# Kernel tuning notes

Measured on AMD Instinct MI355X. Metric: run time of the kernel, lower is better.

Reference implementation:

```python
import jax, jax.numpy as jnp
import numpy as np

NPERSEG = 512
STEP = 256
NSEG = 9            # frames for L=2048 with boundary='zeros', padded=True
NFREQ = 257
NUM_FILTER = 2
PI = 3.1415926      # same constant as source

_win = 0.5 * (1.0 - jnp.cos(2.0 * jnp.pi * jnp.arange(NPERSEG, dtype=jnp.float32) / NPERSEG))  # periodic hann (scipy get_window('hann'))
_win_sum = 256.0    # sum of periodic hann, exact


def _stft(x):
    # x: (B, D, L) real -> scipy.signal.stft(..., nperseg=512, noverlap=256) => (B, D, 257, 9)
    xp = jnp.pad(x, ((0, 0), (0, 0), (STEP, STEP)))  # boundary='zeros'
    idx = jnp.arange(NSEG)[:, None] * STEP + jnp.arange(NPERSEG)[None, :]
    frames = xp[..., idx] * _win                     # (B,D,9,512)
    Z = jnp.fft.rfft(frames, axis=-1) / _win_sum     # scaling='spectrum'
    return jnp.swapaxes(Z, -1, -2)                   # (B,D,257,9)


def _istft(Z):
    # Z: (B,D,257,9) complex -> (B,D,2048) real (scipy.signal.istft inverse)
    xs = jnp.fft.irfft(jnp.swapaxes(Z, -1, -2) * _win_sum, n=NPERSEG, axis=-1) * _win  # (B,D,9,512)
    total = NPERSEG + (NSEG - 1) * STEP  # 2560
    idx = (jnp.arange(NSEG)[:, None] * STEP + jnp.arange(NPERSEG)[None, :]).reshape(-1)
    B, D = Z.shape[0], Z.shape[1]
    x = jnp.zeros((B, D, total), xs.dtype).at[..., idx].add(xs.reshape(B, D, -1))
    norm = jnp.zeros((total,), jnp.float32).at[idx].add(jnp.tile(_win ** 2, NSEG))
    x = x / jnp.where(norm > 1e-10, norm, 1.0)
    return x[..., STEP:total - STEP]  # trim boundary padding -> length 2048


def _cplx(p):
    return p[..., 0] + 1j * p[..., 1]  # torch.view_as_complex


def _filter(x, length, bank):
    # x: (B,S,D) complex; bank: (K,S,D,2). power = x*x/length (complex square, as in source)
    power = x * x / length
    k = jnp.arange(NUM_FILTER, dtype=jnp.float32)
    coef = jnp.cos((2.0 * (k + 1.0) - 1.0) * PI / 2.0 * NUM_FILTER)  # matches source precedence
    return jnp.sum(power[None] * _cplx(bank)[:, None] * coef[:, None, None, None], axis=0)


def _ln(x, g, b):
    m = jnp.mean(x, -1, keepdims=True)
    v = jnp.mean((x - m) ** 2, -1, keepdims=True)
    return (x - m) * jax.lax.rsqrt(v + 1e-5) * g + b


def _addnorm(x, g1, b1, w1, bb1, w2, bb2, g2, b2):
    x = _ln(x, g1, b1)
    h = jax.nn.gelu(x @ w1.T + bb1, approximate=False)  # torch GELU (exact)
    return _ln(h @ w2.T + bb2 + x, g2, b2)


def setup_inputs() -> dict:
    key = jax.random.key(0)
    ks = jax.random.split(key, 12)
    B, D = 8, 768
    d = {}
    d['ecg'] = jax.random.normal(ks[0], (B, 2048, D), jnp.float32)
    d['image'] = jax.random.normal(ks[1], (B, 196, D), jnp.float32)
    d['ecg_filter_bank'] = jax.random.normal(ks[2], (2, 2313, D, 2), jnp.float32)
    d['cxr_filter_bank'] = jax.random.normal(ks[3], (2, 99, D, 2), jnp.float32)
    d['gate_sel'] = jax.random.normal(ks[4], (99, D, 2), jnp.float32)
    d['gate_w'] = jax.random.normal(ks[5], (D, D), jnp.float32) * 0.02
    d['gate_b'] = jnp.zeros((D,), jnp.float32)
    for i, p in enumerate(['e', 'c']):
        d[p + '_ln1_g'] = jnp.ones((D,), jnp.float32)
        d[p + '_ln1_b'] = jnp.zeros((D,), jnp.float32)
        d[p + '_w1'] = jax.random.normal(ks[6 + 2 * i], (D, D), jnp.float32) * 0.02
        d[p + '_b1'] = jnp.zeros((D,), jnp.float32)
        d[p + '_w2'] = jax.random.normal(ks[7 + 2 * i], (D, D), jnp.float32) * 0.02
        d[p + '_b2'] = jnp.zeros((D,), jnp.float32)
        d[p + '_ln2_g'] = jnp.ones((D,), jnp.float32)
        d[p + '_ln2_b'] = jnp.zeros((D,), jnp.float32)
    return d


def reference(ecg, image, ecg_filter_bank, cxr_filter_bank, gate_sel, gate_w, gate_b,
              e_ln1_g, e_ln1_b, e_w1, e_b1, e_w2, e_b2, e_ln2_g, e_ln2_b,
              c_ln1_g, c_ln1_b, c_w1, c_b1, c_w2, c_b2, c_ln2_g, c_ln2_b):
    B, S, D = ecg.shape
    N = image.shape[1]
    # STFT path (source detaches to CPU -> stop_gradient)
    Z = _stft(jnp.swapaxes(jax.lax.stop_gradient(ecg), 1, 2))       # (B,D,257,9)
    _ecg = jnp.transpose(Z, (0, 2, 3, 1)).reshape(B, NFREQ * NSEG, D)
    _img = jnp.fft.rfft(image, axis=1, norm='ortho')                # (B,99,D)
    _ecg = _filter(_ecg, NFREQ * NSEG, ecg_filter_bank)
    _img = _filter(_img, N // 2 + 1, cxr_filter_bank)
    # Cxr2EcgGate: complex selection, avgpool over spatial (real part), 1x1 conv
    gate = jnp.mean((_img * _cplx(gate_sel)).real, axis=1) @ gate_w.T + gate_b  # (B,D)
    ecg_g = _ecg * gate[:, None, :]
    # NOTE: source overwrites gated image with irfft of filtered _image (ecg_gate output unused)
    img_t = jnp.fft.irfft(_img, n=N, axis=1, norm='ortho')          # (B,N,D)
    Zg = jnp.transpose(ecg_g.reshape(B, NFREQ, NSEG, D), (0, 3, 1, 2))
    ecg_t = jnp.swapaxes(_istft(jax.lax.stop_gradient(Zg)), 1, 2)   # (B,2048,D); source detaches before istft
    text = _addnorm(ecg_t + ecg, e_ln1_g, e_ln1_b, e_w1, e_b1, e_w2, e_b2, e_ln2_g, e_ln2_b)
    img = _addnorm(img_t + image, c_ln1_g, c_ln1_b, c_w1, c_b1, c_w2, c_b2, c_ln2_g, c_ln2_b)
    return (text, img)
```

## Files before the change

kernel.cpp:

```cpp
#include <hip/hip_runtime.h>
#include <math.h>

namespace {

constexpr int B_ = 8;
constexpr int S_ = 2048;
constexpr int D_ = 768;
constexpr int N_ = 196;
constexpr int NF_ = 99;
constexpr int NFREQ_ = 257;
constexpr int NSEG_ = 9;
constexpr int NBINS_ = NFREQ_ * NSEG_;
constexpr int NW_ = D_ * D_;
constexpr float TWOPI_ = 6.28318530717958647692f;

using bf16x8 = __attribute__((ext_vector_type(8))) short;
using f32x4  = __attribute__((ext_vector_type(4))) float;

__device__ __forceinline__ int rev9(int x) { return (int)(__brev((unsigned)x) >> 23); }
__device__ __forceinline__ int padz(int i) { return i + (i >> 4); }

__device__ __forceinline__ unsigned short f2bf(float x) {
  unsigned u = __float_as_uint(x);
  u = (u + 0x7FFFu + ((u >> 16) & 1u)) >> 16;
  return (unsigned short)u;
}
__device__ __forceinline__ float bf2f(unsigned short h) {
  return __uint_as_float(((unsigned)h) << 16);
}

__device__ __forceinline__ float gelu_f(float v) {
  const float x = fabsf(v) * 0.70710678118654752440f;
  const float t = 1.0f / fmaf(0.3275911f, x, 1.0f);
  float p = fmaf(fmaf(fmaf(fmaf(1.061405429f, t, -1.453152027f), t, 1.421413741f),
                      t, -0.284496736f), t, 0.254829592f);
  const float e = __expf(-x * x);
  const float er = 1.0f - p * t * e;
  return 0.5f * v * (1.0f + ((v < 0.f) ? -er : er));
}

__device__ __forceinline__ void gload16(const void* g, void* l) {
  __builtin_amdgcn_global_load_lds((const __attribute__((address_space(1))) void*)g,
                                   (__attribute__((address_space(3))) void*)l, 16, 0, 0);
}

__device__ __forceinline__ float2 cmulf(float2 a, float2 b) {
  return make_float2(a.x * b.x - a.y * b.y, a.x * b.y + a.y * b.x);
}
__device__ __forceinline__ float2 cadd(float2 a, float2 b) {
  return make_float2(a.x + b.x, a.y + b.y);
}
__device__ __forceinline__ float2 csub(float2 a, float2 b) {
  return make_float2(a.x - b.x, a.y - b.y);
}

__global__ __launch_bounds__(256) void k_transpose_g(const float* __restrict__ src,
                                                     float* __restrict__ dst,
                                                     int R, int C) {
  __shared__ float tile[32][33];
  const int b = blockIdx.z;
  const int c0 = blockIdx.x * 32;
  const int r0 = blockIdx.y * 32;
  const int tx = threadIdx.x & 31, ty = threadIdx.x >> 5;
  for (int i = ty; i < 32; i += 8)
    tile[i][tx] = src[((size_t)b * R + r0 + i) * C + c0 + tx];
  __syncthreads();
  for (int i = ty; i < 32; i += 8)
    dst[((size_t)b * C + c0 + i) * R + r0 + tx] = tile[tx][i];
}

constexpr int PREP_W = (NW_ + 255) / 256;
constexpr int PREP_WALL = 4 * PREP_W;
__global__ __launch_bounds__(256) void k_prep(
    const float* __restrict__ w0, const float* __restrict__ w1,
    const float* __restrict__ w2, const float* __restrict__ w3,
    unsigned short* __restrict__ wbf, float2* __restrict__ twg,
    float2* __restrict__ twN) {
  const int bid = blockIdx.x;
  if (bid < PREP_WALL) {
    const int m = bid / PREP_W;
    const int i = (bid - m * PREP_W) * 256 + threadIdx.x;
    if (i >= NW_) return;
    const float* src = (m == 0) ? w0 : (m == 1) ? w1 : (m == 2) ? w2 : w3;
    wbf[(size_t)m * NW_ + i] = f2bf(src[i]);
  } else if (bid < PREP_WALL + 2) {
    const int i = (bid - PREP_WALL) * 256 + threadIdx.x;
    if (i >= 511) return;
    const int v = i + 1;
    const int h = 1 << (31 - __clz(v));
    const int j = v - h;
    float sn, cs;
    sincosf((float)j * ((TWOPI_ * 0.5f) / (float)h), &sn, &cs);
    twg[i] = make_float2(cs, sn);
  } else {
    const int i = threadIdx.x;
    if (i >= N_) return;
    float sn, cs;
    sincosf(TWOPI_ * (float)i / (float)N_, &sn, &cs);
    twN[i] = make_float2(cs, sn);
  }
}

__global__ __launch_bounds__(256) void k_fc_t(const float2* __restrict__ e2,
                                              float2* __restrict__ FcT) {
  __shared__ float2 tile[32][33];
  const int d0 = blockIdx.x * 32;
  const int k0 = blockIdx.y * 32;
  const int f = blockIdx.z;
  const int tx = threadIdx.x & 31, ty = threadIdx.x >> 5;
  for (int i = ty; i < 32; i += 8) {
    const int k = k0 + i;
    if (k < NFREQ_) {
      const size_t s = (size_t)(k * 9 + f) * D_ + d0 + tx;
      const float2 a = e2[s];
      const float2 b = e2[(size_t)NBINS_ * D_ + s];
      tile[i][tx] = make_float2(-(a.x + b.x), -(a.y + b.y));
    }
  }
  __syncthreads();
  const int k = k0 + tx;
  if (k < NFREQ_) {
    for (int i = ty; i < 32; i += 8)
      FcT[(size_t)(d0 + i) * NBINS_ + f * 257 + k] = tile[tx][i];
  }
}

__global__ __launch_bounds__(256) void k_img_dft_f(
    const float* __restrict__ image, const float2* __restrict__ bank2,
    const float2* __restrict__ gsel2, const float2* __restrict__ twN,
    float2* __restrict__ imgF, float* __restrict__ part) {
  const int fg = blockIdx.x;
  const int f0 = fg * 9;
  const int d = blockIdx.y * 256 + threadIdx.x;
  const int b = blockIdx.z;
  __shared__ float2 tws[9 * N_];
  for (int idx = threadIdx.x; idx < 9 * N_; idx += 256) {
    const int fi = idx / N_;
    const int t = idx - fi * N_;
    tws[idx] = twN[((f0 + fi) * t) % N_];
  }
  __syncthreads();
  float re[9] = {}, im[9] = {};
  const float* ip = image + (size_t)b * N_ * D_ + d;
  for (int t = 0; t < N_; ++t) {
    const float v = ip[(size_t)t * D_];
#pragma unroll
    for (int fi = 0; fi < 9; ++fi) {
      const float2 w = tws[fi * N_ + t];
      re[fi] = fmaf(v, w.x, re[fi]);
      im[fi] = fmaf(-v, w.y, im[fi]);
    }
  }
  const float sc = 1.0f / (196.0f * 99.0f);
  float gp = 0.f;
#pragma unroll
  for (int fi = 0; fi < 9; ++fi) {
    const int f = f0 + fi;
    const float pr = (re[fi] * re[fi] - im[fi] * im[fi]) * sc;
    const float pi2 = (2.f * re[fi] * im[fi]) * sc;
    const size_t fd = (size_t)f * D_ + d;
    const float2 c0 = bank2[fd];
    const float2 c1 = bank2[(size_t)NF_ * D_ + fd];
    const float fcr = -(c0.x + c1.x), fci = -(c0.y + c1.y);
    const float zr = pr * fcr - pi2 * fci;
    const float zi = pr * fci + pi2 * fcr;
    imgF[(size_t)(b * NF_ + f) * D_ + d] = make_float2(zr, zi);
    const float2 gw = gsel2[fd];
    gp += zr * gw.x - zi * gw.y;
  }
  part[((size_t)b * 11 + fg) * D_ + d] = gp;
}

__global__ __launch_bounds__(256) void k_gate_mm2(const float* __restrict__ part,
                                                  const float* __restrict__ W,
                                                  const float* __restrict__ bias,
                                                  float* __restrict__ gate) {
  __shared__ float row[8][D_];
  __shared__ float red[16][16][8];
  const int tid = threadIdx.x;
  const int d0 = blockIdx.x * 16;
  for (int i = tid; i < 8 * D_; i += 256) {
    const int b = i / D_, e = i - b * D_;
    float s = 0.f;
    for (int p = 0; p < 11; ++p) s += part[((size_t)b * 11 + p) * D_ + e];
    row[b][e] = s * (1.0f / 99.0f);
  }
  __syncthreads();
  const int dl = tid >> 4;
  const int ec = tid & 15;
  const float* w = W + (size_t)(d0 + dl) * D_ + ec * 48;
  float acc[8] = {};
  for (int e = 0; e < 48; e += 4) {
    const float4 wv = *reinterpret_cast<const float4*>(w + e);
    const int eg = ec * 48 + e;
#pragma unroll
    for (int b = 0; b < 8; ++b) {
      acc[b] = fmaf(row[b][eg], wv.x, acc[b]);
      acc[b] = fmaf(row[b][eg + 1], wv.y, acc[b]);
      acc[b] = fmaf(row[b][eg + 2], wv.z, acc[b]);
      acc[b] = fmaf(row[b][eg + 3], wv.w, acc[b]);
    }
  }
#pragma unroll
  for (int b = 0; b < 8; ++b) red[dl][ec][b] = acc[b];
  __syncthreads();
  if (tid < 128) {
    const int dl2 = tid >> 3, b = tid & 7;
    float s = bias[d0 + dl2];
    for (int c = 0; c < 16; ++c) s += red[dl2][c][b];
    gate[b * D_ + d0 + dl2] = s;
  }
}

__global__ __launch_bounds__(256) void k_img_idft(
    const float2* __restrict__ imgF, const float* __restrict__ image,
    const float2* __restrict__ twN, float* __restrict__ xi) {
  const int t0 = blockIdx.x * 14;
  const int d = blockIdx.y * 256 + threadIdx.x;
  const int b = blockIdx.z;
  __shared__ float2 tws[14 * NF_];
  for (int idx = threadIdx.x; idx < 14 * NF_; idx += 256) {
    const int ti = idx / NF_;
    const int f = idx - ti * NF_;
    tws[idx] = twN[((t0 + ti) * f) % N_];
  }
  __syncthreads();
  const float2* zp = imgF + (size_t)b * NF_ * D_ + d;
  const float2 z0 = zp[0];
  const float2 zny = zp[(size_t)(NF_ - 1) * D_];
  float acc[14];
#pragma unroll
  for (int ti = 0; ti < 14; ++ti)
    acc[ti] = z0.x + (((t0 + ti) & 1) ? -zny.x : zny.x);
  for (int f = 1; f < NF_ - 1; ++f) {
    const float2 z = zp[(size_t)f * D_];
#pragma unroll
    for (int ti = 0; ti < 14; ++ti) {
      const float2 w = tws[ti * NF_ + f];
      acc[ti] += 2.f * (z.x * w.x - z.y * w.y);
    }
  }
#pragma unroll
  for (int ti = 0; ti < 14; ++ti) {
    const size_t idx = (size_t)(b * N_ + t0 + ti) * D_ + d;
    xi[idx] = acc[ti] * (1.0f / 14.0f) + image[idx];
  }
}

__global__ __launch_bounds__(256) void k_layernorm_f2b(const float* __restrict__ x,
                                                       const float* __restrict__ g,
                                                       const float* __restrict__ b,
                                                       unsigned short* __restrict__ out) {
  const int row = blockIdx.x;
  const int tid = threadIdx.x;
  const float* xr = x + (size_t)row * D_;
  const float v0 = xr[tid], v1 = xr[tid + 256], v2 = xr[tid + 512];
  float s = v0 + v1 + v2;
  float q = v0 * v0 + v1 * v1 + v2 * v2;
  __shared__ float red[8];
  for (int off = 32; off > 0; off >>= 1) {
    s += __shfl_down(s, off);
    q += __shfl_down(q, off);
  }
  if ((tid & 63) == 0) { red[tid >> 6] = s; red[4 + (tid >> 6)] = q; }
  __syncthreads();
  s = red[0] + red[1] + red[2] + red[3];
  q = red[4] + red[5] + red[6] + red[7];
  const float mean = s * (1.0f / 768.0f);
  const float var = q * (1.0f / 768.0f) - mean * mean;
  const float inv = rsqrtf(var + 1e-5f);
  unsigned short* orow = out + (size_t)row * D_;
  orow[tid]       = f2bf((v0 - mean) * inv * g[tid]       + b[tid]);
  orow[tid + 256] = f2bf((v1 - mean) * inv * g[tid + 256] + b[tid + 256]);
  orow[tid + 512] = f2bf((v2 - mean) * inv * g[tid + 512] + b[tid + 512]);
}

template <int H, int DIR, bool TRIV>
__device__ __forceinline__ void pass8(float2* z, int l,
                                      float2 wa, float2 wb, float2 wc) {
  asm volatile("s_waitcnt lgkmcnt(0)" ::: "memory");
  const float sg = (DIR < 0) ? -1.f : 1.f;
  const int base = (H == 1) ? (l << 3)
                 : (H == 8) ? (((l >> 3) << 6) | (l & 7))
                            : l;
  const float2 x0 = z[padz(base)],         x1 = z[padz(base + H)];
  const float2 x2 = z[padz(base + 2 * H)], x3 = z[padz(base + 3 * H)];
  const float2 x4 = z[padz(base + 4 * H)], x5 = z[padz(base + 5 * H)];
  const float2 x6 = z[padz(base + 6 * H)], x7 = z[padz(base + 7 * H)];
  const float2 WA = make_float2(wa.x, sg * wa.y);
  const float2 WB = make_float2(wb.x, sg * wb.y);
  const float2 WC = make_float2(wc.x, sg * wc.y);
  const float2 WBp = make_float2(-sg * WB.y, sg * WB.x);
  float2 t, u;
  t = TRIV ? x1 : cmulf(x1, WA); const float2 A0 = cadd(x0, t), A1 = csub(x0, t);
  t = TRIV ? x3 : cmulf(x3, WA); const float2 A2 = cadd(x2, t), A3 = csub(x2, t);
  t = TRIV ? x5 : cmulf(x5, WA); const float2 A4 = cadd(x4, t), A5 = csub(x4, t);
  t = TRIV ? x7 : cmulf(x7, WA); const float2 A6 = cadd(x6, t), A7 = csub(x6, t);
  t = TRIV ? A2 : cmulf(A2, WB);
  u = TRIV ? make_float2(-sg * A3.y, sg * A3.x) : cmulf(A3, WBp);
  const float2 B0 = cadd(A0, t), B2 = csub(A0, t);
  const float2 B1 = cadd(A1, u), B3 = csub(A1, u);
  t = TRIV ? A6 : cmulf(A6, WB);
  u = TRIV ? make_float2(-sg * A7.y, sg * A7.x) : cmulf(A7, WBp);
  const float2 B4 = cadd(A4, t), B6 = csub(A4, t);
  const float2 B5 = cadd(A5, u), B7 = csub(A5, u);
  const float r_ = 0.70710678118654752440f;
  const float2 F1 = TRIV ? make_float2(r_, sg * r_)
                         : cmulf(WC, make_float2(r_, sg * r_));
  const float2 F2 = TRIV ? make_float2(0.f, sg)
                         : make_float2(-sg * WC.y, sg * WC.x);
  const float2 F3 = TRIV ? make_float2(-r_, sg * r_)
                         : cmulf(WC, make_float2(-r_, sg * r_));
  t = TRIV ? B4 : cmulf(B4, WC);
  z[padz(base)]         = cadd(B0, t);
  z[padz(base + 4 * H)] = csub(B0, t);
  t = cmulf(B5, F1);
  z[padz(base + H)]     = cadd(B1, t);
  z[padz(base + 5 * H)] = csub(B1, t);
  t = cmulf(B6, F2);
  z[padz(base + 2 * H)] = cadd(B2, t);
  z[padz(base + 6 * H)] = csub(B2, t);
  t = cmulf(B7, F3);
  z[padz(base + 3 * H)] = cadd(B3, t);
  z[padz(base + 7 * H)] = csub(B3, t);
}

template <int FA, int FB>
__device__ __forceinline__ void scatter_buf(float2* z, const float (&s)[8],
                                            float wlo, float whi, int rlo, int rhi) {
  constexpr int iAlo = (FA > 0) ? FA - 1 : 0;
  constexpr int iAhi = (FA < 8) ? FA : 0;
  constexpr int iBlo = (FB > 0) ? FB - 1 : 0;
  constexpr int iBhi = (FB >= 0 && FB < 8) ? FB : 0;
  const float aLo = (FA == 0) ? 0.f : s[iAlo] * wlo;
  const float aHi = (FA == 8) ? 0.f : s[iAhi] * whi;
  const float bLo = (FB <= 0) ? 0.f : s[iBlo] * wlo;
  const float bHi = (FB < 0 || FB == 8) ? 0.f : s[iBhi] * whi;
  z[rlo] = make_float2(aLo, bLo);
  z[rhi] = make_float2(aHi, bHi);
}

template <int FA, int FB>
__device__ __forceinline__ void filt_pack(const float2* z, int k, float g,
                                          float2 cA, float2 cB,
                                          float2& Ck, float2& Cm) {
  const int q = (512 - k) & 511;
  const float2 Zk = z[padz(k)], Zq = z[padz(q)];
  const float sc = 0.5f / 256.f;
  const float ar = (Zk.x + Zq.x) * sc, ai = (Zk.y - Zq.y) * sc;
  float yar, yai, ybr = 0.f, ybi = 0.f;
  {
    const float pr = (ar * ar - ai * ai) * (1.f / 2313.f);
    const float pi = (2.f * ar * ai) * (1.f / 2313.f);
    yar = (pr * cA.x - pi * cA.y) * g;
    yai = (pr * cA.y + pi * cA.x) * g;
  }
  if (FB >= 0) {
    const float br = (Zk.y + Zq.y) * sc, bi = (Zq.x - Zk.x) * sc;
    const float pr = (br * br - bi * bi) * (1.f / 2313.f);
    const float pi = (2.f * br * bi) * (1.f / 2313.f);
    ybr = (pr * cB.x - pi * cB.y) * g;
    ybi = (pr * cB.y + pi * cB.x) * g;
  }
  if (k == 0 || k == 256) {
    Ck = make_float2(yar, ybr);
    Cm = Ck;
  } else {
    Ck = make_float2(yar - ybi, yai + ybr);
    Cm = make_float2(yar + ybi, ybr - yai);
  }
}

template <int FA0, int FB0, int FA1, int FB1, int FA2, int FB2, int FA3, int FB3,
          int NBUF>
__device__ __forceinline__ void ecg_super4(int tid, float g,
                                           const float2* __restrict__ fc,
                                           const float (&s)[8], const float2 (&ptw)[6],
                                           float2 t8, float2* zA, float2* zB,
                                           float2* zC, float2* zD, float* accr) {
  const float c0 = t8.x;
  const float wlo = 0.5f - 0.5f * c0;
  const float whi = 0.5f + 0.5f * c0;
  float2 cA0 = fc[FA0 * 257 + tid];
  float2 cB0 = make_float2(0.f, 0.f), cA1 = cB0, cB1 = cB0;
  float2 cA2 = cB0, cB2 = cB0, cA3 = cB0, cB3 = cB0;
  if (FB0 >= 0) cB0 = fc[FB0 * 257 + tid];
  if (NBUF > 1) { cA1 = fc[FA1 * 257 + tid]; cB1 = fc[FB1 * 257 + tid]; }
  if (NBUF > 2) { cA2 = fc[FA2 * 257 + tid]; cB2 = fc[FB2 * 257 + tid]; }
  if (NBUF > 3) { cA3 = fc[FA3 * 257 + tid]; cB3 = fc[FB3 * 257 + tid]; }
  __syncthreads();
  const int rlo = padz(rev9(tid)), rhi = padz(rev9(tid + 256));
  scatter_buf<FA0, FB0>(zA, s, wlo, whi, rlo, rhi);
  if (NBUF > 1) scatter_buf<FA1, FB1>(zB, s, wlo, whi, rlo, rhi);
  if (NBUF > 2) scatter_buf<FA2, FB2>(zC, s, wlo, whi, rlo, rhi);
  if (NBUF > 3) scatter_buf<FA3, FB3>(zD, s, wlo, whi, rlo, rhi);
  __syncthreads();
  const int wid = tid >> 6, l = tid & 63;
  if (wid < NBUF) {
    float2* zz = (wid == 0) ? zA : (wid == 1) ? zB : (wid == 2) ? zC : zD;
    pass8<1, -1, true>(zz, l, ptw[0], ptw[1], ptw[2]);
    pass8<8, -1, false>(zz, l, ptw[0], ptw[1], ptw[2]);
    pass8<64, -1, false>(zz, l, ptw[3], ptw[4], ptw[5]);
  }
  __syncthreads();
  float2 Ck0, Cm0, Ck1, Cm1, Ck2, Cm2, Ck3, Cm3;
  float2 Cn0, Cn1, Cn2, Cn3, dum;
  filt_pack<FA0, FB0>(zA, tid, g, cA0, cB0, Ck0, Cm0);
  if (NBUF > 1) filt_pack<FA1, FB1>(zB, tid, g, cA1, cB1, Ck1, Cm1);
  if (NBUF > 2) filt_pack<FA2, FB2>(zC, tid, g, cA2, cB2, Ck2, Cm2);
  if (NBUF > 3) filt_pack<FA3, FB3>(zD, tid, g, cA3, cB3, Ck3, Cm3);
  if (tid == 0) {
    float2 nA, nB = make_float2(0.f, 0.f);
    nA = fc[FA0 * 257 + 256];
    if (FB0 >= 0) nB = fc[FB0 * 257 + 256];
    filt_pack<FA0, FB0>(zA, 256, g, nA, nB, Cn0, dum);
    if (NBUF > 1) {
      nA = fc[FA1 * 257 + 256]; nB = fc[FB1 * 257 + 256];
      filt_pack<FA1, FB1>(zB, 256, g, nA, nB, Cn1, dum);
    }
    if (NBUF > 2) {
      nA = fc[FA2 * 257 + 256]; nB = fc[FB2 * 257 + 256];
      filt_pack<FA2, FB2>(zC, 256, g, nA, nB, Cn2, dum);
    }
    if (NBUF > 3) {
      nA = fc[FA3 * 257 + 256]; nB = fc[FB3 * 257 + 256];
      filt_pack<FA3, FB3>(zD, 256, g, nA, nB, Cn3, dum);
    }
  }
  __syncthreads();
  {
    zA[rlo] = Ck0;
    if (NBUF > 1) zB[rlo] = Ck1;
    if (NBUF > 2) zC[rlo] = Ck2;
    if (NBUF > 3) zD[rlo] = Ck3;
    if (tid == 0) {
      zA[padz(1)] = Cn0;
      if (NBUF > 1) zB[padz(1)] = Cn1;
      if (NBUF > 2) zC[padz(1)] = Cn2;
      if (NBUF > 3) zD[padz(1)] = Cn3;
    } else {
      const int rm = padz(rev9(512 - tid));
      zA[rm] = Cm0;
      if (NBUF > 1) zB[rm] = Cm1;
      if (NBUF > 2) zC[rm] = Cm2;
      if (NBUF > 3) zD[rm] = Cm3;
    }
  }
  __syncthreads();
  if (wid < NBUF) {
    float2* zz = (wid == 0) ? zA : (wid == 1) ? zB : (wid == 2) ? zC : zD;
    pass8<1, 1, true>(zz, l, ptw[0], ptw[1], ptw[2]);
    pass8<8, 1, false>(zz, l, ptw[0], ptw[1], ptw[2]);
    pass8<64, 1, false>(zz, l, ptw[3], ptw[4], ptw[5]);
  }
  __syncthreads();
  {
    const float2 vLo = zA[padz(tid)], vHi = zA[padz(tid + 256)];
    accr[FA0] += 0.5f * wlo * vLo.x;
    accr[FA0 + 1] += 0.5f * whi * vHi.x;
    if (FB0 >= 0) {
      accr[FB0] += 0.5f * wlo * vLo.y;
      accr[FB0 + 1] += 0.5f * whi * vHi.y;
    }
    if (NBUF > 1) {
      const float2 uLo = zB[padz(tid)], uHi = zB[padz(tid + 256)];
      accr[FA1] += 0.5f * wlo * uLo.x;
      accr[FA1 + 1] += 0.5f * whi * uHi.x;
      accr[FB1] += 0.5f * wlo * uLo.y;
      accr[FB1 + 1] += 0.5f * whi * uHi.y;
    }
    if (NBUF > 2) {
      const float2 uLo = zC[padz(tid)], uHi = zC[padz(tid + 256)];
      accr[FA2] += 0.5f * wlo * uLo.x;
      accr[FA2 + 1] += 0.5f * whi * uHi.x;
      accr[FB2] += 0.5f * wlo * uLo.y;
      accr[FB2 + 1] += 0.5f * whi * uHi.y;
    }
    if (NBUF > 3) {
      const float2 uLo = zD[padz(tid)], uHi = zD[padz(tid + 256)];
      accr[FA3] += 0.5f * wlo * uLo.x;
      accr[FA3 + 1] += 0.5f * whi * uHi.x;
      accr[FB3] += 0.5f * wlo * uLo.y;
      accr[FB3 + 1] += 0.5f * whi * uHi.y;
    }
  }
}

__global__ __launch_bounds__(256) void k_ecg_fft(
    const float* __restrict__ ecgT, const float2* __restrict__ FcT,
    const float* __restrict__ gate, const float2* __restrict__ twg,
    unsigned short* __restrict__ xtT) {
  const int bd = blockIdx.x;
  const int d = bd % D_;
  const int tid = threadIdx.x;

  __shared__ float2 zA[544], zB[544], zC[544], zD[544];

  float s[8];
  const float* src = ecgT + (size_t)bd * S_;
#pragma unroll
  for (int k = 0; k < 8; ++k) s[k] = src[k * 256 + tid];

  const int l6 = tid & 63;
  float2 ptw[6];
  ptw[0] = twg[7 + (l6 & 7)];
  ptw[1] = twg[15 + (l6 & 7)];
  ptw[2] = twg[31 + (l6 & 7)];
  ptw[3] = twg[63 + l6];
  ptw[4] = twg[127 + l6];
  ptw[5] = twg[255 + l6];
  const float2 t8 = twg[255 + tid];

  const float g = gate[bd];
  const float2* fc = FcT + (size_t)d * NBINS_;
  float accr[10];
#pragma unroll
  for (int i = 0; i < 10; ++i) accr[i] = 0.f;

  ecg_super4<0, 8, 1, 2, 3, 4, 5, 6, 4>(tid, g, fc, s, ptw, t8, zA, zB, zC, zD, accr);
  ecg_super4<7, -1, 0, 0, 0, 0, 0, 0, 1>(tid, g, fc, s, ptw, t8, zA, zB, zC, zD, accr);

  const float c0 = t8.x;
  const float rinv = 1.0f / (0.5f + 0.5f * c0 * c0);
  unsigned short* dst = xtT + (size_t)bd * S_;
#pragma unroll
  for (int i2 = 0; i2 < 8; ++i2)
    dst[i2 * 256 + tid] = f2bf(accr[i2 + 1] * rinv + s[i2]);
}

__global__ __launch_bounds__(256) void k_colstats_bf(const unsigned short* __restrict__ xtT,
                                                     float2* __restrict__ stats) {
  const int b = blockIdx.y;
  const int t0 = blockIdx.x * 128;
  const int tx = threadIdx.x & 63;
  const int ty = threadIdx.x >> 6;
  float s0 = 0.f, q0 = 0.f, s1 = 0.f, q1 = 0.f;
  const unsigned int* base = (const unsigned int*)(xtT + (size_t)b * D_ * S_);
  for (int dd = ty; dd < D_; dd += 4) {
    const unsigned int u = base[(size_t)dd * (S_ / 2) + (t0 >> 1) + tx];
    const float v0 = bf2f((unsigned short)(u & 0xffffu));
    const float v1 = bf2f((unsigned short)(u >> 16));
    s0 += v0; q0 = fmaf(v0, v0, q0);
    s1 += v1; q1 = fmaf(v1, v1, q1);
  }
  __shared__ float sh[4][64][4];
  sh[ty][tx][0] = s0; sh[ty][tx][1] = q0; sh[ty][tx][2] = s1; sh[ty][tx][3] = q1;
  __syncthreads();
  if (ty == 0) {
    s0 = sh[0][tx][0] + sh[1][tx][0] + sh[2][tx][0] + sh[3][tx][0];
    q0 = sh[0][tx][1] + sh[1][tx][1] + sh[2][tx][1] + sh[3][tx][1];
    s1 = sh[0][tx][2] + sh[1][tx][2] + sh[2][tx][2] + sh[3][tx][2];
    q1 = sh[0][tx][3] + sh[1][tx][3] + sh[2][tx][3] + sh[3][tx][3];
    stats[(size_t)b * S_ + t0 + 2 * tx]     = make_float2(s0, q0);
    stats[(size_t)b * S_ + t0 + 2 * tx + 1] = make_float2(s1, q1);
  }
}

__global__ __launch_bounds__(256) void k_transpose_ln(
    const unsigned short* __restrict__ xtT, const float2* __restrict__ stats,
    const float* __restrict__ g, const float* __restrict__ bia,
    unsigned short* __restrict__ xhat) {
  __shared__ float tile[32][33];
  const int b = blockIdx.z;
  const int t0 = blockIdx.x * 32;
  const int d0 = blockIdx.y * 32;
  const int tx = threadIdx.x & 31, ty = threadIdx.x >> 5;
  for (int i = ty; i < 32; i += 8)
    tile[i][tx] = bf2f(xtT[((size_t)b * D_ + d0 + i) * S_ + t0 + tx]);
  __syncthreads();
  const float gv = g[d0 + tx], bv = bia[d0 + tx];
  for (int i = ty; i < 32; i += 8) {
    const float2 st = stats[(size_t)b * S_ + t0 + i];
    const float mean = st.x * (1.0f / 768.0f);
    const float var = st.y * (1.0f / 768.0f) - mean * mean;
    const float inv = rsqrtf(var + 1e-5f);
    xhat[((size_t)b * S_ + t0 + i) * D_ + d0 + tx] =
        f2bf((tile[tx][i] - mean) * inv * gv + bv);
  }
}

__global__ __launch_bounds__(256) void k_layernorm_dual(
    const unsigned short* __restrict__ x1, const float* __restrict__ g1,
    const float* __restrict__ b1, float* __restrict__ o1, int n1,
    const unsigned short* __restrict__ x2, const float* __restrict__ g2,
    const float* __restrict__ b2, float* __restrict__ o2) {
  int row = blockIdx.x;
  const unsigned short* x; const float *g, *b; float* o;
  if (row < n1) { x = x1; g = g1; b = b1; o = o1; }
  else { row -= n1; x = x2; g = g2; b = b2; o = o2; }
  const int tid = threadIdx.x;
  const unsigned short* xr = x + (size_t)row * D_;
  const float v0 = bf2f(xr[tid]), v1 = bf2f(xr[tid + 256]), v2 = bf2f(xr[tid + 512]);
  float s = v0 + v1 + v2;
  float q = v0 * v0 + v1 * v1 + v2 * v2;
  __shared__ float red[8];
  for (int off = 32; off > 0; off >>= 1) {
    s += __shfl_down(s, off);
    q += __shfl_down(q, off);
  }
  if ((tid & 63) == 0) { red[tid >> 6] = s; red[4 + (tid >> 6)] = q; }
  __syncthreads();
  s = red[0] + red[1] + red[2] + red[3];
  q = red[4] + red[5] + red[6] + red[7];
  const float mean = s * (1.0f / 768.0f);
  const float var = q * (1.0f / 768.0f) - mean * mean;
  const float inv = rsqrtf(var + 1e-5f);
  float* orow = o + (size_t)row * D_;
  orow[tid]       = (v0 - mean) * inv * g[tid]       + b[tid];
  orow[tid + 256] = (v1 - mean) * inv * g[tid + 256] + b[tid + 256];
  orow[tid + 512] = (v2 - mean) * inv * g[tid + 512] + b[tid + 512];
}

template <int MODE>
__global__ __launch_bounds__(256) void k_gemm_dual(
    const unsigned short* __restrict__ A1, const unsigned short* __restrict__ W1,
    const float* __restrict__ b1, const unsigned short* __restrict__ r1,
    unsigned short* __restrict__ o1, int M1, int nby1,
    const unsigned short* __restrict__ A2, const unsigned short* __restrict__ W2,
    const float* __restrict__ b2, const unsigned short* __restrict__ r2,
    unsigned short* __restrict__ o2, int M2) {
  __shared__ unsigned short Asm[2][128 * 64];
  __shared__ unsigned short Bsm[2][128 * 64];
  const int tid = threadIdx.x;
  const int lane = tid & 63, wid = tid >> 6;
  const int wr = wid >> 1, wc = wid & 1;
  int bx, by;
  {
    const int nwg = gridDim.x * gridDim.y;
    const int bid = blockIdx.y * gridDim.x + blockIdx.x;
    const int xcd = bid & 7, lin = bid >> 3;
    const int qq = nwg >> 3, rr = nwg & 7;
    const int nbid = (xcd < rr) ? xcd * (qq + 1) + lin
                                : rr * (qq + 1) + (xcd - rr) * qq + lin;
    bx = nbid % gridDim.x;
    by = nbid / gridDim.x;
  }
  const unsigned short* Abf; const unsigned short* Wbf; const float* bias;
  const unsigned short* resid; unsigned short* outb; int M;
  if (by < nby1) { Abf = A1; Wbf = W1; bias = b1; resid = r1; outb = o1; M = M1; }
  else { by -= nby1; Abf = A2; Wbf = W2; bias = b2; resid = r2; outb = o2; M = M2; }
  const int n0 = bx * 128, m0 = by * 128;

  auto STAGE = [&](int buf, int kt) {
    const int k0 = kt * 64;
#pragma unroll
    for (int i = 0; i < 4; ++i) {
      const int c = tid + 256 * i;
      const int row = c >> 3, sl = c & 7;
      const int gsl = sl ^ (row & 7);
      gload16(Abf + (size_t)(m0 + row) * 768 + k0 + gsl * 8, &Asm[buf][c * 8]);
      gload16(Wbf + (size_t)(n0 + row) * 768 + k0 + gsl * 8, &Bsm[buf][c * 8]);
    }
  };

  f32x4 acc[4][4] = {};
  STAGE(0, 0);
  for (int kt = 0; kt < 12; ++kt) {
    const int cur = kt & 1;
    if (kt < 11) {
      STAGE(cur ^ 1, kt + 1);
      asm volatile("s_waitcnt vmcnt(8)" ::: "memory");
    } else {
      asm volatile("s_waitcnt vmcnt(0)" ::: "memory");
    }
    __builtin_amdgcn_sched_barrier(0);
    __builtin_amdgcn_s_barrier();
#pragma unroll
    for (int ks = 0; ks < 2; ++ks) {
      bf16x8 af[4], bfv[4];
#pragma unroll
      for (int mi = 0; mi < 4; ++mi) {
        const int row = wr * 64 + mi * 16 + (lane & 15);
        const int sl = (ks * 4 + (lane >> 4)) ^ (row & 7);
        af[mi] = *(const bf16x8*)((const char*)Asm[cur] + row * 128 + sl * 16);
      }
#pragma unroll
      for (int ni = 0; ni < 4; ++ni) {
        const int row = wc * 64 + ni * 16 + (lane & 15);
        const int sl = (ks * 4 + (lane >> 4)) ^ (row & 7);
        bfv[ni] = *(const bf16x8*)((const char*)Bsm[cur] + row * 128 + sl * 16);
      }
#pragma unroll
      for (int mi = 0; mi < 4; ++mi)
#pragma unroll
        for (int ni = 0; ni < 4; ++ni)
          acc[mi][ni] = __builtin_amdgcn_mfma_f32_16x16x32_bf16(af[mi], bfv[ni],
                                                                acc[mi][ni], 0, 0, 0);
    }
    __builtin_amdgcn_sched_barrier(0);
    __builtin_amdgcn_s_barrier();
  }
#pragma unroll
  for (int mi = 0; mi < 4; ++mi) {
#pragma unroll
    for (int ni = 0; ni < 4; ++ni) {
      const int col = n0 + wc * 64 + ni * 16 + (lane & 15);
#pragma unroll
      for (int e = 0; e < 4; ++e) {
        const int row = m0 + wr * 64 + mi * 16 + (lane >> 4) * 4 + e;
        if (row >= M) continue;
        float v = acc[mi][ni][e] + bias[col];
        if (MODE == 0) {
          v = gelu_f(v);
        } else {
          v += bf2f(resid[(size_t)row * 768 + col]);
        }
        outb[(size_t)row * 768 + col] = f2bf(v);
      }
    }
  }
}

}

extern "C" void kernel_launch(void* const* d_in, const int* in_sizes, int n_in,
                              void* d_out, int out_size, void* d_ws, size_t ws_size,
                              hipStream_t stream) {
  (void)in_sizes; (void)n_in; (void)out_size; (void)ws_size;
  const float* ecg     = (const float*)d_in[0];
  const float* image   = (const float*)d_in[1];
  const float* ebank   = (const float*)d_in[2];
  const float* cbank   = (const float*)d_in[3];
  const float* gsel    = (const float*)d_in[4];
  const float* gw      = (const float*)d_in[5];
  const float* gb      = (const float*)d_in[6];
  const float* e_ln1_g = (const float*)d_in[7];
  const float* e_ln1_b = (const float*)d_in[8];
  const float* e_w1    = (const float*)d_in[9];
  const float* e_b1    = (const float*)d_in[10];
  const float* e_w2    = (const float*)d_in[11];
  const float* e_b2    = (const float*)d_in[12];
  const float* e_ln2_g = (const float*)d_in[13];
  const float* e_ln2_b = (const float*)d_in[14];
  const float* c_ln1_g = (const float*)d_in[15];
  const float* c_ln1_b = (const float*)d_in[16];
  const float* c_w1    = (const float*)d_in[17];
  const float* c_b1    = (const float*)d_in[18];
  const float* c_w2    = (const float*)d_in[19];
  const float* c_b2    = (const float*)d_in[20];
  const float* c_ln2_g = (const float*)d_in[21];
  const float* c_ln2_b = (const float*)d_in[22];

  float* out = (float*)d_out;
  float* ws = (float*)d_ws;

  constexpr size_t TXT = (size_t)8 * 2048 * 768;
  constexpr size_t IMG = (size_t)8 * 196 * 768;

  float* A  = ws;
  float* Bb = A + TXT;
  unsigned short* wbf = (unsigned short*)(Bb + TXT);
  unsigned short* ew1b = wbf;
  unsigned short* ew2b = wbf + NW_;
  unsigned short* cw1b = wbf + 2 * NW_;
  unsigned short* cw2b = wbf + 3 * NW_;
  float* gatev = (float*)(wbf + 4 * (size_t)NW_);
  float2* stats = (float2*)(gatev + 8 * 768);
  float* gpart = (float*)(stats + 8 * 2048);
  float2* twg = (float2*)(gpart + 8 * 11 * 768);
  float2* twN = twg + 511;

  float2* FcT = (float2*)out;

  unsigned short* xhat = (unsigned short*)A;
  unsigned short* y_tb = (unsigned short*)A + TXT;
  unsigned short* xtT = (unsigned short*)Bb;
  unsigned short* h_t = (unsigned short*)Bb;
  float* Bb2 = Bb + TXT / 2;
  float2* imgF = (float2*)Bb2;
  float* xi = Bb2 + 1216512;
  unsigned short* xh_i = (unsigned short*)(xi + IMG);
  unsigned short* h_i  = xh_i + IMG;
  unsigned short* y_ib = h_i + IMG;

  k_prep<<<PREP_WALL + 3, 256, 0, stream>>>(e_w1, e_w2, c_w1, c_w2, wbf, twg, twN);
  k_fc_t<<<dim3(24, 9, 9), 256, 0, stream>>>((const float2*)ebank, FcT);

  k_img_dft_f<<<dim3(11, 3, 8), 256, 0, stream>>>(image, (const float2*)cbank,
                                                  (const float2*)gsel, twN, imgF, gpart);
  k_gate_mm2<<<48, 256, 0, stream>>>(gpart, gw, gb, gatev);
  k_img_idft<<<dim3(14, 3, 8), 256, 0, stream>>>(imgF, image, twN, xi);
  k_layernorm_f2b<<<1568, 256, 0, stream>>>(xi, c_ln1_g, c_ln1_b, xh_i);

  k_transpose_g<<<dim3(24, 64, 8), 256, 0, stream>>>(ecg, A, 2048, 768);
  k_ecg_fft<<<8 * 768, 256, 0, stream>>>(A, FcT, gatev, twg, xtT);
  k_colstats_bf<<<dim3(16, 8), 256, 0, stream>>>(xtT, stats);
  k_transpose_ln<<<dim3(64, 24, 8), 256, 0, stream>>>(xtT, stats, e_ln1_g, e_ln1_b, xhat);

  k_gemm_dual<0><<<dim3(6, 141), 256, 0, stream>>>(
      xhat, ew1b, e_b1, nullptr, h_t, 16384, 128,
      xh_i, cw1b, c_b1, nullptr, h_i, 1568);
  k_gemm_dual<1><<<dim3(6, 141), 256, 0, stream>>>(
      h_t, ew2b, e_b2, xhat, y_tb, 16384, 128,
      h_i, cw2b, c_b2, xh_i, y_ib, 1568);
  k_layernorm_dual<<<16384 + 1568, 256, 0, stream>>>(
      y_tb, e_ln2_g, e_ln2_b, out, 16384,
      y_ib, c_ln2_g, c_ln2_b, out + TXT);
}
```

Baseline: 389.9 us.

## Process two ECG channels per block to pack the leftover frame FFT

The ECG STFT/iSTFT kernel now handles two adjacent channels per block. The four-buffer super-pass runs for each channel, and the ninth (odd-one-out) frame of both channels is packed into one complex FFT, with per-channel gates applied separately in the filter step. This halves the grid and removes the mostly idle single-wave pass that each channel previously ran alone. In exchange it raises register pressure from two sets of sample and accumulator arrays, which may lower occupancy.

```diff
diff --git a/kernel.cpp b/kernel.cpp
--- a/kernel.cpp
+++ b/kernel.cpp
@@ -341,9 +341,9 @@
 }
 
 template <int FA, int FB>
-__device__ __forceinline__ void filt_pack(const float2* z, int k, float g,
-                                          float2 cA, float2 cB,
-                                          float2& Ck, float2& Cm) {
+__device__ __forceinline__ void filt_pack2(const float2* z, int k, float gA, float gB,
+                                           float2 cA, float2 cB,
+                                           float2& Ck, float2& Cm) {
   const int q = (512 - k) & 511;
   const float2 Zk = z[padz(k)], Zq = z[padz(q)];
   const float sc = 0.5f / 256.f;
@@ -352,15 +352,15 @@
   {
     const float pr = (ar * ar - ai * ai) * (1.f / 2313.f);
     const float pi = (2.f * ar * ai) * (1.f / 2313.f);
-    yar = (pr * cA.x - pi * cA.y) * g;
-    yai = (pr * cA.y + pi * cA.x) * g;
+    yar = (pr * cA.x - pi * cA.y) * gA;
+    yai = (pr * cA.y + pi * cA.x) * gA;
   }
   if (FB >= 0) {
     const float br = (Zk.y + Zq.y) * sc, bi = (Zq.x - Zk.x) * sc;
     const float pr = (br * br - bi * bi) * (1.f / 2313.f);
     const float pi = (2.f * br * bi) * (1.f / 2313.f);
-    ybr = (pr * cB.x - pi * cB.y) * g;
-    ybi = (pr * cB.y + pi * cB.x) * g;
+    ybr = (pr * cB.x - pi * cB.y) * gB;
+    ybi = (pr * cB.y + pi * cB.x) * gB;
   }
   if (k == 0 || k == 256) {
     Ck = make_float2(yar, ybr);
@@ -405,26 +405,26 @@
   __syncthreads();
   float2 Ck0, Cm0, Ck1, Cm1, Ck2, Cm2, Ck3, Cm3;
   float2 Cn0, Cn1, Cn2, Cn3, dum;
-  filt_pack<FA0, FB0>(zA, tid, g, cA0, cB0, Ck0, Cm0);
-  if (NBUF > 1) filt_pack<FA1, FB1>(zB, tid, g, cA1, cB1, Ck1, Cm1);
-  if (NBUF > 2) filt_pack<FA2, FB2>(zC, tid, g, cA2, cB2, Ck2, Cm2);
-  if (NBUF > 3) filt_pack<FA3, FB3>(zD, tid, g, cA3, cB3, Ck3, Cm3);
+  filt_pack2<FA0, FB0>(zA, tid, g, g, cA0, cB0, Ck0, Cm0);
+  if (NBUF > 1) filt_pack2<FA1, FB1>(zB, tid, g, g, cA1, cB1, Ck1, Cm1);
+  if (NBUF > 2) filt_pack2<FA2, FB2>(zC, tid, g, g, cA2, cB2, Ck2, Cm2);
+  if (NBUF > 3) filt_pack2<FA3, FB3>(zD, tid, g, g, cA3, cB3, Ck3, Cm3);
   if (tid == 0) {
     float2 nA, nB = make_float2(0.f, 0.f);
     nA = fc[FA0 * 257 + 256];
     if (FB0 >= 0) nB = fc[FB0 * 257 + 256];
-    filt_pack<FA0, FB0>(zA, 256, g, nA, nB, Cn0, dum);
+    filt_pack2<FA0, FB0>(zA, 256, g, g, nA, nB, Cn0, dum);
     if (NBUF > 1) {
       nA = fc[FA1 * 257 + 256]; nB = fc[FB1 * 257 + 256];
-      filt_pack<FA1, FB1>(zB, 256, g, nA, nB, Cn1, dum);
+      filt_pack2<FA1, FB1>(zB, 256, g, g, nA, nB, Cn1, dum);
     }
     if (NBUF > 2) {
       nA = fc[FA2 * 257 + 256]; nB = fc[FB2 * 257 + 256];
-      filt_pack<FA2, FB2>(zC, 256, g, nA, nB, Cn2, dum);
+      filt_pack2<FA2, FB2>(zC, 256, g, g, nA, nB, Cn2, dum);
     }
     if (NBUF > 3) {
       nA = fc[FA3 * 257 + 256]; nB = fc[FB3 * 257 + 256];
-      filt_pack<FA3, FB3>(zD, 256, g, nA, nB, Cn3, dum);
+      filt_pack2<FA3, FB3>(zD, 256, g, g, nA, nB, Cn3, dum);
     }
   }
   __syncthreads();
@@ -490,16 +490,19 @@
     const float* __restrict__ ecgT, const float2* __restrict__ FcT,
     const float* __restrict__ gate, const float2* __restrict__ twg,
     unsigned short* __restrict__ xtT) {
-  const int bd = blockIdx.x;
-  const int d = bd % D_;
+  const int bp = blockIdx.x;
+  const int b = bp / 384, dp = bp - (bp / 384) * 384;
+  const int dX = 2 * dp;
+  const int bdX = b * D_ + dX;
   const int tid = threadIdx.x;
 
   __shared__ float2 zA[544], zB[544], zC[544], zD[544];
 
-  float s[8];
-  const float* src = ecgT + (size_t)bd * S_;
-#pragma unroll
-  for (int k = 0; k < 8; ++k) s[k] = src[k * 256 + tid];
+  float sX[8], sY[8];
+  const float* srcX = ecgT + (size_t)bdX * S_;
+  const float* srcY = srcX + S_;
+#pragma unroll
+  for (int k = 0; k < 8; ++k) { sX[k] = srcX[k * 256 + tid]; sY[k] = srcY[k * 256 + tid]; }
 
   const int l6 = tid & 63;
   float2 ptw[6];
@@ -510,22 +513,74 @@
   ptw[4] = twg[127 + l6];
   ptw[5] = twg[255 + l6];
   const float2 t8 = twg[255 + tid];
-
-  const float g = gate[bd];
-  const float2* fc = FcT + (size_t)d * NBINS_;
-  float accr[10];
-#pragma unroll
-  for (int i = 0; i < 10; ++i) accr[i] = 0.f;
-
-  ecg_super4<0, 8, 1, 2, 3, 4, 5, 6, 4>(tid, g, fc, s, ptw, t8, zA, zB, zC, zD, accr);
-  ecg_super4<7, -1, 0, 0, 0, 0, 0, 0, 1>(tid, g, fc, s, ptw, t8, zA, zB, zC, zD, accr);
-
   const float c0 = t8.x;
+  const float wlo = 0.5f - 0.5f * c0;
+  const float whi = 0.5f + 0.5f * c0;
+  const int rlo = padz(rev9(tid)), rhi = padz(rev9(tid + 256));
+
+  const float gX = gate[bdX];
+  const float gY = gate[bdX + 1];
+  const float2* fcX = FcT + (size_t)dX * NBINS_;
+  const float2* fcY = fcX + NBINS_;
+
+  float accX[10], accY[10];
+#pragma unroll
+  for (int i = 0; i < 10; ++i) { accX[i] = 0.f; accY[i] = 0.f; }
+
+  ecg_super4<0, 8, 1, 2, 3, 4, 5, 6, 4>(tid, gX, fcX, sX, ptw, t8, zA, zB, zC, zD, accX);
+  ecg_super4<0, 8, 1, 2, 3, 4, 5, 6, 4>(tid, gY, fcY, sY, ptw, t8, zA, zB, zC, zD, accY);
+
+  __syncthreads();
+  zA[rlo] = make_float2(sX[6] * wlo, sY[6] * wlo);
+  zA[rhi] = make_float2(sX[7] * whi, sY[7] * whi);
+  __syncthreads();
+  const int wid = tid >> 6, l = tid & 63;
+  if (wid == 0) {
+    pass8<1, -1, true>(zA, l, ptw[0], ptw[1], ptw[2]);
+    pass8<8, -1, false>(zA, l, ptw[0], ptw[1], ptw[2]);
+    pass8<64, -1, false>(zA, l, ptw[3], ptw[4], ptw[5]);
+  }
+  __syncthreads();
+  float2 CkC, CmC, CnC, dum;
+  {
+    const float2 cA = fcX[7 * 257 + tid];
+    const float2 cB = fcY[7 * 257 + tid];
+    filt_pack2<7, 7>(zA, tid, gX, gY, cA, cB, CkC, CmC);
+    if (tid == 0) {
+      const float2 nA = fcX[7 * 257 + 256];
+      const float2 nB = fcY[7 * 257 + 256];
+      filt_pack2<7, 7>(zA, 256, gX, gY, nA, nB, CnC, dum);
+    }
+  }
+  __syncthreads();
+  {
+    zA[rlo] = CkC;
+    if (tid == 0) zA[padz(1)] = CnC;
+    else zA[padz(rev9(512 - tid))] = CmC;
+  }
+  __syncthreads();
+  if (wid == 0) {
+    pass8<1, 1, true>(zA, l, ptw[0], ptw[1], ptw[2]);
+    pass8<8, 1, false>(zA, l, ptw[0], ptw[1], ptw[2]);
+    pass8<64, 1, false>(zA, l, ptw[3], ptw[4], ptw[5]);
+  }
+  __syncthreads();
+  {
+    const float2 vLo = zA[padz(tid)], vHi = zA[padz(tid + 256)];
+    accX[7] += 0.5f * wlo * vLo.x;
+    accX[8] += 0.5f * whi * vHi.x;
+    accY[7] += 0.5f * wlo * vLo.y;
+    accY[8] += 0.5f * whi * vHi.y;
+  }
+
   const float rinv = 1.0f / (0.5f + 0.5f * c0 * c0);
-  unsigned short* dst = xtT + (size_t)bd * S_;
-#pragma unroll
-  for (int i2 = 0; i2 < 8; ++i2)
-    dst[i2 * 256 + tid] = f2bf(accr[i2 + 1] * rinv + s[i2]);
+  unsigned short* dstX = xtT + (size_t)bdX * S_;
+  unsigned short* dstY = dstX + S_;
+#pragma unroll
+  for (int i2 = 0; i2 < 8; ++i2) {
+    dstX[i2 * 256 + tid] = f2bf(accX[i2 + 1] * rinv + sX[i2]);
+    dstY[i2 * 256 + tid] = f2bf(accY[i2 + 1] * rinv + sY[i2]);
+  }
 }
 
 __global__ __launch_bounds__(256) void k_colstats_bf(const unsigned short* __restrict__ xtT,
@@ -783,7 +838,7 @@
   k_layernorm_f2b<<<1568, 256, 0, stream>>>(xi, c_ln1_g, c_ln1_b, xh_i);
 
   k_transpose_g<<<dim3(24, 64, 8), 256, 0, stream>>>(ecg, A, 2048, 768);
-  k_ecg_fft<<<8 * 768, 256, 0, stream>>>(A, FcT, gatev, twg, xtT);
+  k_ecg_fft<<<3072, 256, 0, stream>>>(A, FcT, gatev, twg, xtT);
   k_colstats_bf<<<dim3(16, 8), 256, 0, stream>>>(xtT, stats);
   k_transpose_ln<<<dim3(64, 24, 8), 256, 0, stream>>>(xtT, stats, e_ln1_g, e_ln1_b, xhat);
 
```

New measurement: 390.8 us. About the same (+0.2%).
